# Performance work log

Measured on AMD Instinct MI355X. Metric: run time of the kernel, lower is better.

Reference implementation:

```python
import jax, jax.numpy as jnp
import numpy as np

NUM_CHANNELS = 32
NUM_GRIDS = 2048
BATCH = 32
MIN_XI = 0.1
MAX_XI = 5.0
DX = 0.08


def setup_inputs() -> dict:
    key = jax.random.key(0)
    k1, k2 = jax.random.split(key)
    inputs = jax.random.normal(k1, (BATCH, NUM_GRIDS), dtype=jnp.float32)
    # uniform real-space grid, centered at 0, spacing DX
    grids = (jnp.arange(NUM_GRIDS, dtype=jnp.float32) - NUM_GRIDS / 2) * DX
    # eta initialized ~ N(0, 1e-4) as in the original RandomNormal(0, 0.0001)
    eta = 0.0001 * jax.random.normal(k2, (NUM_CHANNELS,), dtype=jnp.float32)
    return {"inputs": inputs, "grids": grids, "eta": eta}


def reference(inputs, grids, eta):
    # widths in (MIN_XI, MAX_XI) via sigmoid reparameterization, shape (C,)
    widths = MIN_XI + (MAX_XI - MIN_XI) * jax.nn.sigmoid(eta)
    # pairwise displacements |x_n - x_m|, shape (N, N)
    absdisp = jnp.abs(grids[:, None] - grids[None, :])
    # exponential (Laplace) kernels, shape (N, N, C)
    kernels = jnp.exp(-absdisp[:, :, None] / widths) / (2.0 * widths)
    # tensordot(inputs, kernels, axes=(1, 0)) -> (B, N, C), scaled by dx
    return jnp.einsum("bn,nmc->bmc", inputs, kernels) * DX
```

## Files before the change

### kernel.cpp

```cpp
#include <hip/hip_runtime.h>
#include <math.h>

namespace {

constexpr int NCH   = 32;
constexpr int NG    = 2048;
constexpr int BATCH = 32;
constexpr float DXC = 0.08f;

constexpr int NSEG   = 8;
constexpr int SEGLEN = NG / NSEG;
constexpr int NCHUNK = 32;
constexpr int CHL    = NG / NCHUNK;
constexpr int NSUB   = 8;
constexpr int SUBL   = CHL / NSUB;
constexpr int CPS    = NCHUNK / NSEG;

__global__ __launch_bounds__(1024)
void egc_kernel(const float* __restrict__ inputs,
                const float* __restrict__ eta,
                float* __restrict__ out) {
    __shared__ float xs[NG];
    __shared__ float F8[CPS][NSUB][NCH];
    __shared__ float G8[CPS][NSUB][NCH];
    __shared__ float Ef[NCHUNK][NCH];
    __shared__ float Eb[NCHUNK][NCH];
    __shared__ float CF[NCHUNK][NCH];
    __shared__ float CB[NCHUNK][NCH];

    const int tid = threadIdx.x;
    const int c   = tid & 31;
    const int t   = tid >> 5;
    const int bid = blockIdx.x;
    const int b   = bid >> 3;
    const int seg = bid & (NSEG - 1);

    const float e   = eta[c];
    const float sig = 1.0f / (1.0f + expf(-e));
    const float w   = 0.1f + 4.9f * sig;
    const float lam = DXC / w;
    const float r   = expf(-lam);
    const float s   = 0.5f * DXC / w;

    const float* xrow = inputs + (size_t)b * NG;
    xs[tid]        = xrow[tid];
    xs[tid + 1024] = xrow[tid + 1024];
    __syncthreads();

    {
        const int base = t * CHL;
        const int tc   = t - seg * CPS;
        const bool own = (tc >= 0) && (tc < CPS);
        float f = 0.0f;
#pragma unroll
        for (int i = 0; i < CHL; ++i) {
            f = fmaf(r, f, xs[base + i]);
            if ((i & (SUBL - 1)) == SUBL - 1) {
                if (own) F8[tc][i >> 3][c] = f;
            }
        }
        Ef[t][c] = f;
        float g = 0.0f;
#pragma unroll
        for (int i = CHL - 1; i >= 0; --i) {
            g = fmaf(r, g, xs[base + i]);
            if ((i & (SUBL - 1)) == 0) {
                if (own) G8[tc][i >> 3][c] = g;
            }
        }
        Eb[t][c] = g;
    }
    __syncthreads();

    {
        const float rho = expf(-lam * (float)CHL);
        if (t == 0) {
            float fe = 0.0f;
            for (int k = 0; k < NCHUNK; ++k) {
                CF[k][c] = fe;
                fe = fmaf(rho, fe, Ef[k][c]);
            }
        } else if (t == 2) {
            float ge = 0.0f;
            for (int k = NCHUNK - 1; k >= 0; --k) {
                CB[k][c] = ge;
                ge = fmaf(rho, ge, Eb[k][c]);
            }
        }
    }
    __syncthreads();

    const int T     = seg * (SEGLEN / SUBL) + t;
    const int chunk = T >> 3;
    const int sub   = T & (NSUB - 1);
    const int tc    = chunk - seg * CPS;
    const int m0    = T * SUBL;

    float fin = CF[chunk][c] * expf(-lam * (float)(SUBL * sub));
    if (sub > 0) fin += F8[tc][sub - 1][c];
    float gin;
    if (sub < NSUB - 1)
        gin = G8[tc][sub + 1][c] + CB[chunk][c] * expf(-lam * (float)(CHL - SUBL * (sub + 1)));
    else
        gin = CB[chunk][c];

    float xv[SUBL], Fv[SUBL];
#pragma unroll
    for (int i = 0; i < SUBL; ++i) xv[i] = xs[m0 + i];

    float f = fin;
#pragma unroll
    for (int i = 0; i < SUBL; ++i) { f = fmaf(r, f, xv[i]); Fv[i] = f; }

    float g = gin;
    float* orow = out + (size_t)b * NG * NCH;
#pragma unroll
    for (int i = SUBL - 1; i >= 0; --i) {
        g = fmaf(r, g, xv[i]);
        orow[(size_t)(m0 + i) * NCH + c] = s * (Fv[i] + g - xv[i]);
    }
}

}

extern "C" void kernel_launch(void* const* d_in, const int* in_sizes, int n_in,
                              void* d_out, int out_size, void* d_ws, size_t ws_size,
                              hipStream_t stream) {
    const float* inputs = (const float*)d_in[0];
    const float* eta    = (const float*)d_in[2];
    float* out          = (float*)d_out;

    dim3 grid(BATCH * NSEG);
    dim3 block(1024);
    hipLaunchKernelGGL(egc_kernel, grid, block, 0, stream, inputs, eta, out);
}
```

Before: 61.23 us.

## Break serial chunk scan into independent sub-block dot products with power table

Replaces the 64-step serial recurrence per chunk with 8 independent 8-element weighted sums that use a precomputed shared table of decay powers, followed by a short 8-step combine. This shortens the dependent FMA chain and exposes instruction-level parallelism. The carry scan is unrolled into registers, and per-thread expf calls in the final phase become table lookups. The cost is the extra shared table and more register pressure at 1024 threads per block.

```diff
diff --git a/kernel.cpp b/kernel.cpp
--- a/kernel.cpp
+++ b/kernel.cpp
@@ -21,6 +21,7 @@
                 const float* __restrict__ eta,
                 float* __restrict__ out) {
     __shared__ float xs[NG];
+    __shared__ float pw[64][NCH];
     __shared__ float F8[CPS][NSUB][NCH];
     __shared__ float G8[CPS][NSUB][NCH];
     __shared__ float Ef[NCHUNK][NCH];
@@ -31,61 +32,81 @@
     const int tid = threadIdx.x;
     const int c   = tid & 31;
     const int t   = tid >> 5;
-    const int bid = blockIdx.x;
-    const int b   = bid >> 3;
-    const int seg = bid & (NSEG - 1);
+    const int b   = blockIdx.x >> 3;
+    const int seg = blockIdx.x & (NSEG - 1);
 
     const float e   = eta[c];
     const float sig = 1.0f / (1.0f + expf(-e));
     const float w   = 0.1f + 4.9f * sig;
     const float lam = DXC / w;
-    const float r   = expf(-lam);
     const float s   = 0.5f * DXC / w;
 
     const float* xrow = inputs + (size_t)b * NG;
     xs[tid]        = xrow[tid];
     xs[tid + 1024] = xrow[tid + 1024];
+    pw[t][c]      = expf(-lam * (float)t);
+    pw[t + 32][c] = expf(-lam * (float)(t + 32));
     __syncthreads();
+
+    float p[SUBL];
+#pragma unroll
+    for (int i = 0; i < SUBL; ++i) p[i] = pw[i][c];
+    const float r  = p[1];
+    const float p8 = pw[SUBL][c];
 
     {
         const int base = t * CHL;
-        const int tc   = t - seg * CPS;
+        float sf[NSUB], sb[NSUB];
+#pragma unroll
+        for (int ss = 0; ss < NSUB; ++ss) {
+            const int o = base + ss * SUBL;
+            float xv[SUBL];
+#pragma unroll
+            for (int i = 0; i < SUBL; ++i) xv[i] = xs[o + i];
+            float f = 0.0f, g = 0.0f;
+#pragma unroll
+            for (int i = 0; i < SUBL; ++i) {
+                f = fmaf(p[SUBL - 1 - i], xv[i], f);
+                g = fmaf(p[i],            xv[i], g);
+            }
+            sf[ss] = f; sb[ss] = g;
+        }
+
+        const int  tc  = t - seg * CPS;
         const bool own = (tc >= 0) && (tc < CPS);
-        float f = 0.0f;
+        float fa = 0.0f;
 #pragma unroll
-        for (int i = 0; i < CHL; ++i) {
-            f = fmaf(r, f, xs[base + i]);
-            if ((i & (SUBL - 1)) == SUBL - 1) {
-                if (own) F8[tc][i >> 3][c] = f;
-            }
+        for (int ss = 0; ss < NSUB; ++ss) {
+            fa = fmaf(p8, fa, sf[ss]);
+            if (own) F8[tc][ss][c] = fa;
         }
-        Ef[t][c] = f;
-        float g = 0.0f;
+        float ga = 0.0f;
 #pragma unroll
-        for (int i = CHL - 1; i >= 0; --i) {
-            g = fmaf(r, g, xs[base + i]);
-            if ((i & (SUBL - 1)) == 0) {
-                if (own) G8[tc][i >> 3][c] = g;
-            }
+        for (int ss = NSUB - 1; ss >= 0; --ss) {
+            ga = fmaf(p8, ga, sb[ss]);
+            if (own) G8[tc][ss][c] = ga;
         }
-        Eb[t][c] = g;
+        Ef[t][c] = fa;
+        Eb[t][c] = ga;
     }
     __syncthreads();
 
     {
         const float rho = expf(-lam * (float)CHL);
         if (t == 0) {
+            float ev[NCHUNK];
+#pragma unroll
+            for (int k = 0; k < NCHUNK; ++k) ev[k] = Ef[k][c];
             float fe = 0.0f;
-            for (int k = 0; k < NCHUNK; ++k) {
-                CF[k][c] = fe;
-                fe = fmaf(rho, fe, Ef[k][c]);
-            }
+#pragma unroll
+            for (int k = 0; k < NCHUNK; ++k) { CF[k][c] = fe; fe = fmaf(rho, fe, ev[k]); }
         } else if (t == 2) {
+            float ev[NCHUNK];
+#pragma unroll
+            for (int k = 0; k < NCHUNK; ++k) ev[k] = Eb[k][c];
             float ge = 0.0f;
-            for (int k = NCHUNK - 1; k >= 0; --k) {
-                CB[k][c] = ge;
-                ge = fmaf(rho, ge, Eb[k][c]);
-            }
+#pragma unroll
+            for (int k = NCHUNK - 1; k >= 0; --k) { CB[k][c] = ge; ge = fmaf(rho, ge, ev[k]); }
         }
     }
     __syncthreads();
@@ -96,11 +117,11 @@
     const int tc    = chunk - seg * CPS;
     const int m0    = T * SUBL;
 
-    float fin = CF[chunk][c] * expf(-lam * (float)(SUBL * sub));
+    float fin = CF[chunk][c] * pw[SUBL * sub][c];
     if (sub > 0) fin += F8[tc][sub - 1][c];
     float gin;
     if (sub < NSUB - 1)
-        gin = G8[tc][sub + 1][c] + CB[chunk][c] * expf(-lam * (float)(CHL - SUBL * (sub + 1)));
+        gin = G8[tc][sub + 1][c] + CB[chunk][c] * pw[CHL - SUBL * (sub + 1)][c];
     else
         gin = CB[chunk][c];
 
@@ -113,11 +134,11 @@
     for (int i = 0; i < SUBL; ++i) { f = fmaf(r, f, xv[i]); Fv[i] = f; }
 
     float g = gin;
-    float* orow = out + (size_t)b * NG * NCH;
+    float* orow = out + ((size_t)b * NG + m0) * NCH + c;
 #pragma unroll
     for (int i = SUBL - 1; i >= 0; --i) {
         g = fmaf(r, g, xv[i]);
-        orow[(size_t)(m0 + i) * NCH + c] = s * (Fv[i] + g - xv[i]);
+        orow[(size_t)i * NCH] = s * (Fv[i] + g - xv[i]);
     }
 }
 
```

After: 62.09 us. Within noise of the previous version (+1.4%).
